# Kernel optimization log

Hardware: AMD Instinct MI355X
Metric: run time of the kernel (lower is better)

Reference implementation:

```python
import jax, jax.numpy as jnp
import numpy as np

N_NODES = 50000
N_EDGES = 1000000
HID = 64
L = 3
EPS_MSG = 1e-7   # GENConv message eps
EPS_SM = 1e-16   # PyG scatter-softmax denominator eps
LN_EPS = 1e-5


def layernorm(x, g, b):
    mu = jnp.mean(x, axis=-1, keepdims=True)
    var = jnp.var(x, axis=-1, keepdims=True)
    return (x - mu) * jax.lax.rsqrt(var + LN_EPS) * g + b


def genconv(x, src, dst, edge_attr, t, W1, b1, g1, be1, W2, b2):
    # message: relu(x_j + e_ij) + eps  -> [E, HID]
    msg = jax.nn.relu(x[src] + edge_attr) + EPS_MSG
    # softmax aggregation over incoming edges of each dst node
    logits = msg * t
    m = jax.ops.segment_max(logits, dst, num_segments=N_NODES)
    m = jnp.where(jnp.isfinite(m), m, 0.0)
    e = jnp.exp(logits - m[dst])
    s = jax.ops.segment_sum(e, dst, num_segments=N_NODES) + EPS_SM
    agg = jax.ops.segment_sum((e / s[dst]) * msg, dst, num_segments=N_NODES)
    # root residual + MLP [64 -> 128 -> 64]
    h = agg + x
    h = h @ W1 + b1
    h = jax.nn.relu(layernorm(h, g1, be1))
    return h @ W2 + b2


def setup_inputs() -> dict:
    key = jax.random.key(0)
    ks = jax.random.split(key, 10)
    inp = {
        'x': jax.random.normal(ks[0], (N_NODES, 16), jnp.float32),
        'edge_attr': jax.random.uniform(ks[1], (N_EDGES, 1), jnp.float32),
        'edge_index': jax.random.randint(ks[2], (2, N_EDGES), 0, N_NODES, jnp.int32),
        'W_node': jax.random.normal(ks[3], (16, HID), jnp.float32) / np.sqrt(16.0),
        'b_node': jnp.zeros((HID,), jnp.float32),
        'W_edge': jax.random.normal(ks[4], (1, HID), jnp.float32),
        'b_edge': jnp.zeros((HID,), jnp.float32),
        't': jnp.ones((L,), jnp.float32),
        'W1': jax.random.normal(ks[5], (L, HID, 2 * HID), jnp.float32) / np.sqrt(float(HID)),
        'b1': jnp.zeros((L, 2 * HID), jnp.float32),
        'ln_g': jnp.ones((L, 2 * HID), jnp.float32),
        'ln_b': jnp.zeros((L, 2 * HID), jnp.float32),
        'W2': jax.random.normal(ks[6], (L, 2 * HID, HID), jnp.float32) / np.sqrt(2.0 * HID),
        'b2': jnp.zeros((L, HID), jnp.float32),
        'norm_g': jnp.ones((L, HID), jnp.float32),
        'norm_b': jnp.zeros((L, HID), jnp.float32),
        'W_lin': jax.random.normal(ks[7], (HID, 64), jnp.float32) / np.sqrt(float(HID)),
        'b_lin': jnp.zeros((64,), jnp.float32),
    }
    return inp


def reference(x, edge_attr, edge_index, W_node, b_node, W_edge, b_edge, t,
              W1, b1, ln_g, ln_b, W2, b2, norm_g, norm_b, W_lin, b_lin):
    src, dst = edge_index[0], edge_index[1]
    h = x @ W_node + b_node                 # [N, HID]
    ea = edge_attr @ W_edge + b_edge        # [E, HID]
    # layer 0: conv only
    h = genconv(h, src, dst, ea, t[0], W1[0], b1[0], ln_g[0], ln_b[0], W2[0], b2[0])
    # layers 1..L-1: res+ blocks (norm -> relu -> conv -> residual); dropout is identity in eval
    for i in range(1, L):
        z = jax.nn.relu(layernorm(h, norm_g[i], norm_b[i]))
        h = h + genconv(z, src, dst, ea, t[i], W1[i], b1[i], ln_g[i], ln_b[i], W2[i], b2[i])
    # final norm/act reuses layer 0's norm
    h = jax.nn.relu(layernorm(h, norm_g[0], norm_b[0]))
    # adaptive avg/max pool (N, 64) -> (1, 32): pool over all nodes, channel bins of 2
    avg = h.mean(axis=0).reshape(32, 2).mean(axis=1)
    mx = h.max(axis=0).reshape(32, 2).max(axis=1)
    emb = jnp.concatenate([avg, mx])[None, :]   # [1, 64]
    return emb @ W_lin + b_lin                  # [1, 64]
```

## Files before the change

kernel.cpp:

```cpp
#include <hip/hip_runtime.h>
#include <math.h>

#define N_NODES 50000
#define N_EDGES 1000000
#define HID 64
#define SCAN_NB ((N_NODES + 1 + 255) / 256)
#define N_TILES (N_NODES / 16)
#define NB_MLP 512
#define NB2 64
#define VB_S 72
#define UB_S 136
static_assert(N_NODES % 16 == 0, "tile math");
static_assert(N_NODES <= 65536, "src must fit in 16 bits");

typedef __attribute__((ext_vector_type(8))) short short8;
typedef __attribute__((ext_vector_type(4))) float f32x4;

__device__ __forceinline__ unsigned short f2bf(float x) {
    unsigned u = __float_as_uint(x);
    u += 0x7FFFu + ((u >> 16) & 1u);
    return (unsigned short)(u >> 16);
}
__device__ __forceinline__ float bfbits_hi(unsigned pk) {
    return __uint_as_float(pk & 0xFFFF0000u);
}
__device__ __forceinline__ float bf2f(unsigned short v) {
    return __uint_as_float(((unsigned)v) << 16);
}
__device__ __forceinline__ unsigned addpk(unsigned a, unsigned b) {
    float lo = __uint_as_float(a << 16) + __uint_as_float(b << 16);
    float hi = __uint_as_float(a & 0xFFFF0000u) + __uint_as_float(b & 0xFFFF0000u);
    return (unsigned)f2bf(lo) | ((unsigned)f2bf(hi) << 16);
}

__global__ __launch_bounds__(256) void k_node_encode(
    const float* __restrict__ x, const float* __restrict__ Wn,
    const float* __restrict__ bn, unsigned short* __restrict__ zb) {
    int n = blockIdx.x * 4 + (threadIdx.x >> 6);
    int c = threadIdx.x & 63;
    if (n >= N_NODES) return;
    float acc = bn[c];
    const float* xr = x + n * 16;
    #pragma unroll
    for (int k = 0; k < 16; ++k) acc = fmaf(xr[k], Wn[k * 64 + c], acc);
    zb[n * 64 + c] = f2bf(acc);
}

__global__ __launch_bounds__(256) void k_wprep(
    const float* __restrict__ W1, const float* __restrict__ W2,
    unsigned short* __restrict__ w1p, unsigned short* __restrict__ w2p) {
    int i = blockIdx.x * 256 + threadIdx.x;
    if (i >= 3 * 8192) return;
    int L = i >> 13, r = i & 8191;
    int j = r & 7, lane = (r >> 3) & 63;
    int quad = lane >> 4, col = lane & 15;
    {
        int st = r >> 9;
        int s = st >> 3, t = st & 7;
        w1p[i] = f2bf(W1[L * 8192 + (s * 32 + quad * 8 + j) * 128 + t * 16 + col]);
    }
    {
        int ft = r >> 9;
        int s = ft >> 2, t = ft & 3;
        w2p[i] = f2bf(W2[L * 8192 + (s * 32 + quad * 8 + j) * 64 + t * 16 + col]);
    }
}

__global__ __launch_bounds__(256) void k_hist_rank(const int* __restrict__ ei,
                                                   int* __restrict__ cnt4, int* __restrict__ rank) {
    int i = blockIdx.x * blockDim.x + threadIdx.x;
    if (i >= N_EDGES) return;
    int c = i & 3;
    rank[i] = atomicAdd(&cnt4[c * N_NODES + ei[N_EDGES + i]], 1);
}

__global__ __launch_bounds__(256) void k_scan1(const int* __restrict__ cnt4,
                                               int* __restrict__ tot,
                                               int* __restrict__ inc, int* __restrict__ bsum) {
    __shared__ int sh[256];
    int gi = blockIdx.x * 256 + threadIdx.x;
    int v = 0;
    if (gi < N_NODES)
        v = cnt4[gi] + cnt4[N_NODES + gi] + cnt4[2 * N_NODES + gi] + cnt4[3 * N_NODES + gi];
    if (gi < N_NODES + 1) tot[gi] = v;
    sh[threadIdx.x] = v;
    __syncthreads();
    #pragma unroll
    for (int d = 1; d < 256; d <<= 1) {
        int t = (threadIdx.x >= d) ? sh[threadIdx.x - d] : 0;
        __syncthreads();
        sh[threadIdx.x] += t;
        __syncthreads();
    }
    if (gi < N_NODES + 1) inc[gi] = sh[threadIdx.x];
    if (threadIdx.x == 255) bsum[blockIdx.x] = sh[255];
}

__global__ __launch_bounds__(256) void k_scan2(int* __restrict__ bsum) {
    __shared__ int sh[256];
    int t = threadIdx.x;
    sh[t] = (t < SCAN_NB) ? bsum[t] : 0;
    __syncthreads();
    #pragma unroll
    for (int d = 1; d < 256; d <<= 1) {
        int v = (t >= d) ? sh[t - d] : 0;
        __syncthreads();
        sh[t] += v;
        __syncthreads();
    }
    if (t < SCAN_NB) bsum[t] = (t == 0) ? 0 : sh[t - 1];
}

__global__ __launch_bounds__(256) void k_scan3(const int* __restrict__ inc,
                                               const int* __restrict__ tot,
                                               const int* __restrict__ bsum,
                                               const int* __restrict__ cnt4,
                                               int* __restrict__ offs, int4* __restrict__ combined) {
    int gi = blockIdx.x * 256 + threadIdx.x;
    if (gi < N_NODES + 1) {
        int e = bsum[blockIdx.x] + inc[gi] - tot[gi];
        offs[gi] = e;
        if (gi < N_NODES) {
            int c0 = cnt4[gi], c1 = cnt4[N_NODES + gi], c2 = cnt4[2 * N_NODES + gi];
            combined[gi] = make_int4(e, e + c0, e + c0 + c1, e + c0 + c1 + c2);
        }
    }
}

__global__ __launch_bounds__(256) void k_scatter(
    const int* __restrict__ ei, const float* __restrict__ eattr,
    const int4* __restrict__ combined, const int* __restrict__ rank,
    unsigned int* __restrict__ s_pack) {
    int i = blockIdx.x * blockDim.x + threadIdx.x;
    if (i >= N_EDGES) return;
    int d = ei[N_EDGES + i];
    int c = i & 3;
    int4 cb = combined[d];
    int base = (c == 0) ? cb.x : (c == 1) ? cb.y : (c == 2) ? cb.z : cb.w;
    int p = base + rank[i];
    unsigned pk = ((unsigned)f2bf(eattr[i]) << 16) | (unsigned)(ei[i] & 0xFFFF);
    s_pack[p] = pk;
}

__global__ __launch_bounds__(256) void k_agg(
    const unsigned short* __restrict__ zb, const int* __restrict__ offs,
    const unsigned int* __restrict__ s_pack,
    const float* __restrict__ We, const float* __restrict__ be,
    const float* __restrict__ t, int layer, unsigned short* __restrict__ aggb) {
    int wid = (blockIdx.x * blockDim.x + threadIdx.x) >> 6;
    int lane = threadIdx.x & 63;
    if (wid >= N_NODES) return;
    int beg = offs[wid], end = offs[wid + 1];
    float we = We[lane], bev = be[lane];
    float tl = t[layer];
    float s = 0.f, num = 0.f;
    int i = beg;
    for (; i + 7 < end; i += 8) {
        unsigned pk[8];
        #pragma unroll
        for (int j = 0; j < 8; ++j) pk[j] = s_pack[i + j];
        float zv[8];
        #pragma unroll
        for (int j = 0; j < 8; ++j) zv[j] = bf2f(zb[(pk[j] & 0xFFFFu) * 64 + lane]);
        float acc_s = 0.f, acc_n = 0.f;
        #pragma unroll
        for (int j = 0; j < 8; ++j) {
            float msg = fmaxf(zv[j] + fmaf(bfbits_hi(pk[j]), we, bev), 0.f) + 1e-7f;
            float p = __expf(msg * tl);
            acc_s += p;
            acc_n = fmaf(p, msg, acc_n);
        }
        s += acc_s;
        num += acc_n;
    }
    for (; i < end; ++i) {
        unsigned pk = s_pack[i];
        float zz = bf2f(zb[(pk & 0xFFFFu) * 64 + lane]);
        float msg = fmaxf(zz + fmaf(bfbits_hi(pk), we, bev), 0.f) + 1e-7f;
        float p = __expf(msg * tl);
        s += p;
        num = fmaf(p, msg, num);
    }
    aggb[wid * 64 + lane] = f2bf(num / (s + 1e-16f));
}

__global__ __launch_bounds__(256) void k_mlp(
    const unsigned short* __restrict__ aggb, unsigned short* __restrict__ zb,
    unsigned short* __restrict__ hb,
    const unsigned short* __restrict__ w1p, const unsigned short* __restrict__ w2p,
    const float* __restrict__ b1,
    const float* __restrict__ g1, const float* __restrict__ be1,
    const float* __restrict__ b2,
    const float* __restrict__ ng, const float* __restrict__ nb, int mode,
    float* __restrict__ pb_sum, float* __restrict__ pb_max) {
    __shared__ unsigned short w1s[8192];
    __shared__ unsigned short w2s[8192];
    __shared__ unsigned short vbuf[4][16 * VB_S];
    __shared__ unsigned short ubuf[4][16 * UB_S];
    __shared__ float lssum[4][4][16], lsmax[4][4][16];
    int lane = threadIdx.x & 63;
    int wave = threadIdx.x >> 6;
    int col = lane & 15, quad = lane >> 4;
    unsigned short* vb = vbuf[wave];
    unsigned short* ub = ubuf[wave];

    {
        const uint4* s1 = (const uint4*)w1p;
        const uint4* s2 = (const uint4*)w2p;
        uint4* d1 = (uint4*)w1s;
        uint4* d2 = (uint4*)w2s;
        #pragma unroll
        for (int i = 0; i < 4; ++i) {
            d1[threadIdx.x + i * 256] = s1[threadIdx.x + i * 256];
            d2[threadIdx.x + i * 256] = s2[threadIdx.x + i * 256];
        }
    }
    __syncthreads();

    float b1f[8], g1f[8], e1f[8];
    #pragma unroll
    for (int t = 0; t < 8; ++t) {
        int ch = t * 16 + col;
        b1f[t] = b1[ch]; g1f[t] = g1[ch]; e1f[t] = be1[ch];
    }
    float b2f_[4], ngf[4], nbf[4];
    #pragma unroll
    for (int t = 0; t < 4; ++t) {
        b2f_[t] = b2[t * 16 + col];
        ngf[t] = ng[t * 16 + col];
        nbf[t] = nb[t * 16 + col];
    }

    float psum[4] = {0.f, 0.f, 0.f, 0.f};
    float pmax[4] = {0.f, 0.f, 0.f, 0.f};
    int nd = lane >> 2;
    int cg = (lane & 3) * 16;

    for (int tile = blockIdx.x * 4 + wave; tile < N_TILES; tile += NB_MLP * 4) {
        int n0 = tile * 16;
        const uint4* ap = (const uint4*)(aggb + (size_t)(n0 + nd) * 64 + cg);
        const uint4* zp = (const uint4*)(zb + (size_t)(n0 + nd) * 64 + cg);
        uint4 a0 = ap[0], a1 = ap[1], z0 = zp[0], z1 = zp[1];
        uint4 r0, r1;
        r0.x = addpk(a0.x, z0.x); r0.y = addpk(a0.y, z0.y);
        r0.z = addpk(a0.z, z0.z); r0.w = addpk(a0.w, z0.w);
        r1.x = addpk(a1.x, z1.x); r1.y = addpk(a1.y, z1.y);
        r1.z = addpk(a1.z, z1.z); r1.w = addpk(a1.w, z1.w);
        uint4* vdst = (uint4*)&vb[nd * VB_S + cg];
        vdst[0] = r0;
        vdst[1] = r1;

        short8 af0 = *(const short8*)&vb[col * VB_S + quad * 8];
        short8 af1 = *(const short8*)&vb[col * VB_S + 32 + quad * 8];

        uint4 h0, h1;
        if (mode >= 1) {
            const uint4* hp = (const uint4*)(hb + (size_t)(n0 + nd) * 64 + cg);
            h0 = hp[0]; h1 = hp[1];
        }

        f32x4 au[8];
        #pragma unroll
        for (int t = 0; t < 8; ++t) {
            short8 w0 = *(const short8*)&w1s[((0 * 8 + t) * 64 + lane) * 8];
            short8 w1 = *(const short8*)&w1s[((1 * 8 + t) * 64 + lane) * 8];
            f32x4 c = {0.f, 0.f, 0.f, 0.f};
            c = __builtin_amdgcn_mfma_f32_16x16x32_bf16(af0, w0, c, 0, 0, 0);
            c = __builtin_amdgcn_mfma_f32_16x16x32_bf16(af1, w1, c, 0, 0, 0);
            au[t] = c;
        }
        #pragma unroll
        for (int r = 0; r < 4; ++r) {
            float sx = 0.f, sq = 0.f;
            #pragma unroll
            for (int t = 0; t < 8; ++t) {
                float v = au[t][r] + b1f[t];
                sx += v; sq += v * v;
            }
            #pragma unroll
            for (int mask = 1; mask < 16; mask <<= 1) {
                sx += __shfl_xor(sx, mask, 64);
                sq += __shfl_xor(sq, mask, 64);
            }
            float mu = sx * (1.f / 128.f);
            float var = sq * (1.f / 128.f) - mu * mu;
            float rs = rsqrtf(var + 1e-5f);
            int row = quad * 4 + r;
            #pragma unroll
            for (int t = 0; t < 8; ++t) {
                float v = au[t][r] + b1f[t];
                float y = fmaxf(fmaf((v - mu) * rs, g1f[t], e1f[t]), 0.f);
                ub[row * UB_S + t * 16 + col] = f2bf(y);
            }
        }
        f32x4 oc[4];
        #pragma unroll
        for (int t = 0; t < 4; ++t) oc[t] = (f32x4){0.f, 0.f, 0.f, 0.f};
        #pragma unroll
        for (int s = 0; s < 4; ++s) {
            short8 a = *(const short8*)&ub[col * UB_S + s * 32 + quad * 8];
            #pragma unroll
            for (int t = 0; t < 4; ++t) {
                short8 w = *(const short8*)&w2s[((s * 4 + t) * 64 + lane) * 8];
                oc[t] = __builtin_amdgcn_mfma_f32_16x16x32_bf16(a, w, oc[t], 0, 0, 0);
            }
        }
        if (mode >= 1) {
            uint4* hdst = (uint4*)&vb[nd * VB_S + cg];
            hdst[0] = h0;
            hdst[1] = h1;
        }
        #pragma unroll
        for (int r = 0; r < 4; ++r) {
            int row = quad * 4 + r;
            float val[4];
            #pragma unroll
            for (int t = 0; t < 4; ++t) {
                val[t] = oc[t][r] + b2f_[t];
                if (mode >= 1) val[t] += bf2f(vb[row * VB_S + t * 16 + col]);
            }
            float sx = 0.f, sq = 0.f;
            #pragma unroll
            for (int t = 0; t < 4; ++t) { sx += val[t]; sq += val[t] * val[t]; }
            #pragma unroll
            for (int mask = 1; mask < 16; mask <<= 1) {
                sx += __shfl_xor(sx, mask, 64);
                sq += __shfl_xor(sq, mask, 64);
            }
            float mu = sx * (1.f / 64.f);
            float var = sq * (1.f / 64.f) - mu * mu;
            float rs = rsqrtf(var + 1e-5f);
            #pragma unroll
            for (int t = 0; t < 4; ++t) {
                float y = fmaxf(fmaf((val[t] - mu) * rs, ngf[t], nbf[t]), 0.f);
                if (mode <= 1) {
                    vb[row * VB_S + t * 16 + col] = f2bf(val[t]);
                    ub[row * UB_S + t * 16 + col] = f2bf(y);
                } else {
                    psum[t] += y;
                    pmax[t] = fmaxf(pmax[t], y);
                }
            }
        }
        if (mode <= 1) {
            const uint4* hsrc = (const uint4*)&vb[nd * VB_S + cg];
            const uint4* zsrc = (const uint4*)&ub[nd * UB_S + cg];
            uint4* hdst = (uint4*)(hb + (size_t)(n0 + nd) * 64 + cg);
            uint4* zdst = (uint4*)(zb + (size_t)(n0 + nd) * 64 + cg);
            hdst[0] = hsrc[0]; hdst[1] = hsrc[1];
            zdst[0] = zsrc[0]; zdst[1] = zsrc[1];
        }
    }
    if (mode == 2) {
        #pragma unroll
        for (int t = 0; t < 4; ++t) {
            psum[t] += __shfl_xor(psum[t], 16, 64);
            psum[t] += __shfl_xor(psum[t], 32, 64);
            pmax[t] = fmaxf(pmax[t], __shfl_xor(pmax[t], 16, 64));
            pmax[t] = fmaxf(pmax[t], __shfl_xor(pmax[t], 32, 64));
        }
        if (quad == 0) {
            #pragma unroll
            for (int t = 0; t < 4; ++t) {
                lssum[wave][t][col] = psum[t];
                lsmax[wave][t][col] = pmax[t];
            }
        }
        __syncthreads();
        if (wave == 0) {
            int t = lane >> 4, c = lane & 15;
            float s = lssum[0][t][c] + lssum[1][t][c] + lssum[2][t][c] + lssum[3][t][c];
            float mx = fmaxf(fmaxf(lsmax[0][t][c], lsmax[1][t][c]),
                             fmaxf(lsmax[2][t][c], lsmax[3][t][c]));
            pb_sum[blockIdx.x * 64 + lane] = s;
            pb_max[blockIdx.x * 64 + lane] = mx;
        }
    }
}

__global__ __launch_bounds__(256) void k_red(
    const float* __restrict__ pb_sum, const float* __restrict__ pb_max,
    float* __restrict__ p2_sum, float* __restrict__ p2_max) {
    __shared__ float sa4[4][64], sm4[4][64];
    int t = threadIdx.x;
    int ch = t & 63, part = t >> 6;
    float s = 0.f, mx = 0.f;
    for (int b = blockIdx.x + NB2 * part; b < NB_MLP; b += NB2 * 4) {
        s += pb_sum[b * 64 + ch];
        mx = fmaxf(mx, pb_max[b * 64 + ch]);
    }
    sa4[part][ch] = s; sm4[part][ch] = mx;
    __syncthreads();
    if (t < 64) {
        p2_sum[blockIdx.x * 64 + t] = sa4[0][t] + sa4[1][t] + sa4[2][t] + sa4[3][t];
        p2_max[blockIdx.x * 64 + t] =
            fmaxf(fmaxf(sm4[0][t], sm4[1][t]), fmaxf(sm4[2][t], sm4[3][t]));
    }
}

__global__ __launch_bounds__(256) void k_head(
    const float* __restrict__ p2_sum, const float* __restrict__ p2_max,
    const float* __restrict__ Wl, const float* __restrict__ bl, float* __restrict__ out) {
    __shared__ float sa4[4][64], sm4[4][64];
    __shared__ float sa[64], sm[64], emb[64];
    int t = threadIdx.x;
    int ch = t & 63, part = t >> 6;
    float s = 0.f, mx = 0.f;
    for (int b = part; b < NB2; b += 4) {
        s += p2_sum[b * 64 + ch];
        mx = fmaxf(mx, p2_max[b * 64 + ch]);
    }
    sa4[part][ch] = s; sm4[part][ch] = mx;
    __syncthreads();
    if (t < 64) {
        sa[t] = sa4[0][t] + sa4[1][t] + sa4[2][t] + sa4[3][t];
        sm[t] = fmaxf(fmaxf(sm4[0][t], sm4[1][t]), fmaxf(sm4[2][t], sm4[3][t]));
    }
    __syncthreads();
    if (t < 64) {
        if (t < 32) {
            emb[t] = (sa[2 * t] + sa[2 * t + 1]) * (0.5f / (float)N_NODES);
        } else {
            int i = t - 32;
            emb[t] = fmaxf(sm[2 * i], sm[2 * i + 1]);
        }
    }
    __syncthreads();
    if (t < 64) {
        float acc = bl[t];
        for (int k = 0; k < 64; ++k) acc = fmaf(emb[k], Wl[k * 64 + t], acc);
        out[t] = acc;
    }
}

extern "C" void kernel_launch(void* const* d_in, const int* in_sizes, int n_in,
                              void* d_out, int out_size, void* d_ws, size_t ws_size,
                              hipStream_t stream) {
    const float* x     = (const float*)d_in[0];
    const float* eattr = (const float*)d_in[1];
    const int*   ei    = (const int*)d_in[2];
    const float* Wn    = (const float*)d_in[3];
    const float* bn    = (const float*)d_in[4];
    const float* We    = (const float*)d_in[5];
    const float* be    = (const float*)d_in[6];
    const float* t     = (const float*)d_in[7];
    const float* W1    = (const float*)d_in[8];
    const float* b1    = (const float*)d_in[9];
    const float* lg    = (const float*)d_in[10];
    const float* lb    = (const float*)d_in[11];
    const float* W2    = (const float*)d_in[12];
    const float* b2    = (const float*)d_in[13];
    const float* ng    = (const float*)d_in[14];
    const float* nb    = (const float*)d_in[15];
    const float* Wl    = (const float*)d_in[16];
    const float* bl    = (const float*)d_in[17];
    float* out = (float*)d_out;

    char* p = (char*)d_ws;
    unsigned short* hb   = (unsigned short*)p; p += (size_t)N_NODES * 64 * 2;
    unsigned short* zb   = (unsigned short*)p; p += (size_t)N_NODES * 64 * 2;
    unsigned short* aggb = (unsigned short*)p; p += (size_t)N_NODES * 64 * 2;
    unsigned int* s_pack = (unsigned int*)p; p += (size_t)N_EDGES * 4;
    int* cnt4   = (int*)p;  p += (size_t)4 * N_NODES * 4;
    int* tot    = (int*)p;  p += (size_t)(N_NODES + 4) * 4;
    int* offs   = (int*)p;  p += (size_t)(N_NODES + 4) * 4;
    int* inc    = (int*)p;  p += (size_t)(N_NODES + 4) * 4;
    int* bsum   = (int*)p;  p += (size_t)256 * 4;
    int4* combined = (int4*)p; p += (size_t)N_NODES * 16;
    float* pb_sum = (float*)p; p += (size_t)NB_MLP * 64 * 4;
    float* pb_max = (float*)p; p += (size_t)NB_MLP * 64 * 4;
    float* p2_sum = (float*)p; p += (size_t)NB2 * 64 * 4;
    float* p2_max = (float*)p; p += (size_t)NB2 * 64 * 4;
    unsigned short* w1p = (unsigned short*)p; p += (size_t)3 * 8192 * 2;
    unsigned short* w2p = (unsigned short*)p; p += (size_t)3 * 8192 * 2;
    int* rank = (int*)p;    p += (size_t)N_EDGES * 4;

    hipMemsetAsync(cnt4, 0, (size_t)4 * N_NODES * sizeof(int), stream);

    k_node_encode<<<(N_NODES + 3) / 4, 256, 0, stream>>>(x, Wn, bn, zb);
    k_wprep<<<(3 * 8192 + 255) / 256, 256, 0, stream>>>(W1, W2, w1p, w2p);
    k_hist_rank<<<(N_EDGES + 255) / 256, 256, 0, stream>>>(ei, cnt4, rank);
    k_scan1<<<SCAN_NB, 256, 0, stream>>>(cnt4, tot, inc, bsum);
    k_scan2<<<1, 256, 0, stream>>>(bsum);
    k_scan3<<<SCAN_NB, 256, 0, stream>>>(inc, tot, bsum, cnt4, offs, combined);
    k_scatter<<<(N_EDGES + 255) / 256, 256, 0, stream>>>(ei, eattr, combined, rank, s_pack);

    k_agg<<<(N_NODES + 3) / 4, 256, 0, stream>>>(zb, offs, s_pack, We, be, t, 0, aggb);
    k_mlp<<<NB_MLP, 256, 0, stream>>>(aggb, zb, hb, w1p, w2p, b1, lg, lb, b2,
                                      ng + 64, nb + 64, 0, pb_sum, pb_max);
    k_agg<<<(N_NODES + 3) / 4, 256, 0, stream>>>(zb, offs, s_pack, We, be, t, 1, aggb);
    k_mlp<<<NB_MLP, 256, 0, stream>>>(aggb, zb, hb, w1p + 8192, w2p + 8192,
                                      b1 + 128, lg + 128, lb + 128, b2 + 64,
                                      ng + 128, nb + 128, 1, pb_sum, pb_max);
    k_agg<<<(N_NODES + 3) / 4, 256, 0, stream>>>(zb, offs, s_pack, We, be, t, 2, aggb);
    k_mlp<<<NB_MLP, 256, 0, stream>>>(aggb, zb, hb, w1p + 2 * 8192, w2p + 2 * 8192,
                                      b1 + 2 * 128, lg + 2 * 128, lb + 2 * 128, b2 + 2 * 64,
                                      ng, nb, 2, pb_sum, pb_max);

    k_red<<<NB2, 256, 0, stream>>>(pb_sum, pb_max, p2_sum, p2_max);
    k_head<<<1, 256, 0, stream>>>(p2_sum, p2_max, Wl, bl, out);
}
```

Before: 352.0 us.

## Fuse front kernels, scan stages, pooling reduce; vectorize agg gather over channel pairs

Merges node encoding, weight packing and the edge histogram into one launch, folds the block-sum scan into the final scan kernel, and merges the two-stage pooling reduction into a single 1024-thread head kernel. The aggregation kernel now has each lane process two channels via 32-bit bf16-pair loads, with the two half-waves handling alternating edges and combining through a cross-half shuffle. This reduces launch overhead and per-edge gather instruction count, at the cost of redundant scan work per block and a single-block final reduction.

```diff
diff --git a/kernel.cpp b/kernel.cpp
--- a/kernel.cpp
+++ b/kernel.cpp
@@ -7,9 +7,11 @@
 #define SCAN_NB ((N_NODES + 1 + 255) / 256)
 #define N_TILES (N_NODES / 16)
 #define NB_MLP 512
-#define NB2 64
 #define VB_S 72
 #define UB_S 136
+#define NB_ENC ((N_NODES + 3) / 4)
+#define NB_WPREP ((3 * 8192 + 255) / 256)
+#define NB_HIST ((N_EDGES + 255) / 256)
 static_assert(N_NODES % 16 == 0, "tile math");
 static_assert(N_NODES <= 65536, "src must fit in 16 bits");
 
@@ -33,45 +35,44 @@
     return (unsigned)f2bf(lo) | ((unsigned)f2bf(hi) << 16);
 }
 
-__global__ __launch_bounds__(256) void k_node_encode(
+__global__ __launch_bounds__(256) void k_front(
     const float* __restrict__ x, const float* __restrict__ Wn,
-    const float* __restrict__ bn, unsigned short* __restrict__ zb) {
-    int n = blockIdx.x * 4 + (threadIdx.x >> 6);
-    int c = threadIdx.x & 63;
-    if (n >= N_NODES) return;
-    float acc = bn[c];
-    const float* xr = x + n * 16;
-    #pragma unroll
-    for (int k = 0; k < 16; ++k) acc = fmaf(xr[k], Wn[k * 64 + c], acc);
-    zb[n * 64 + c] = f2bf(acc);
-}
-
-__global__ __launch_bounds__(256) void k_wprep(
+    const float* __restrict__ bn, unsigned short* __restrict__ zb,
     const float* __restrict__ W1, const float* __restrict__ W2,
-    unsigned short* __restrict__ w1p, unsigned short* __restrict__ w2p) {
-    int i = blockIdx.x * 256 + threadIdx.x;
-    if (i >= 3 * 8192) return;
-    int L = i >> 13, r = i & 8191;
-    int j = r & 7, lane = (r >> 3) & 63;
-    int quad = lane >> 4, col = lane & 15;
-    {
-        int st = r >> 9;
-        int s = st >> 3, t = st & 7;
-        w1p[i] = f2bf(W1[L * 8192 + (s * 32 + quad * 8 + j) * 128 + t * 16 + col]);
-    }
-    {
-        int ft = r >> 9;
-        int s = ft >> 2, t = ft & 3;
-        w2p[i] = f2bf(W2[L * 8192 + (s * 32 + quad * 8 + j) * 64 + t * 16 + col]);
-    }
-}
-
-__global__ __launch_bounds__(256) void k_hist_rank(const int* __restrict__ ei,
-                                                   int* __restrict__ cnt4, int* __restrict__ rank) {
-    int i = blockIdx.x * blockDim.x + threadIdx.x;
-    if (i >= N_EDGES) return;
-    int c = i & 3;
-    rank[i] = atomicAdd(&cnt4[c * N_NODES + ei[N_EDGES + i]], 1);
+    unsigned short* __restrict__ w1p, unsigned short* __restrict__ w2p,
+    const int* __restrict__ ei, int* __restrict__ cnt4, int* __restrict__ rank) {
+    int b = blockIdx.x;
+    if (b < NB_ENC) {
+        int n = b * 4 + (threadIdx.x >> 6);
+        int c = threadIdx.x & 63;
+        if (n >= N_NODES) return;
+        float acc = bn[c];
+        const float* xr = x + n * 16;
+        #pragma unroll
+        for (int k = 0; k < 16; ++k) acc = fmaf(xr[k], Wn[k * 64 + c], acc);
+        zb[n * 64 + c] = f2bf(acc);
+    } else if (b < NB_ENC + NB_WPREP) {
+        int i = (b - NB_ENC) * 256 + threadIdx.x;
+        if (i >= 3 * 8192) return;
+        int L = i >> 13, r = i & 8191;
+        int j = r & 7, lane = (r >> 3) & 63;
+        int quad = lane >> 4, col = lane & 15;
+        {
+            int st = r >> 9;
+            int s = st >> 3, t = st & 7;
+            w1p[i] = f2bf(W1[L * 8192 + (s * 32 + quad * 8 + j) * 128 + t * 16 + col]);
+        }
+        {
+            int ft = r >> 9;
+            int s = ft >> 2, t = ft & 3;
+            w2p[i] = f2bf(W2[L * 8192 + (s * 32 + quad * 8 + j) * 64 + t * 16 + col]);
+        }
+    } else {
+        int i = (b - NB_ENC - NB_WPREP) * 256 + threadIdx.x;
+        if (i >= N_EDGES) return;
+        int c = i & 3;
+        rank[i] = atomicAdd(&cnt4[c * N_NODES + ei[N_EDGES + i]], 1);
+    }
 }
 
 __global__ __launch_bounds__(256) void k_scan1(const int* __restrict__ cnt4,
@@ -96,7 +97,11 @@
     if (threadIdx.x == 255) bsum[blockIdx.x] = sh[255];
 }
 
-__global__ __launch_bounds__(256) void k_scan2(int* __restrict__ bsum) {
+__global__ __launch_bounds__(256) void k_scan3(const int* __restrict__ inc,
+                                               const int* __restrict__ tot,
+                                               const int* __restrict__ bsum,
+                                               const int* __restrict__ cnt4,
+                                               int* __restrict__ offs, int4* __restrict__ combined) {
     __shared__ int sh[256];
     int t = threadIdx.x;
     sh[t] = (t < SCAN_NB) ? bsum[t] : 0;
@@ -108,17 +113,10 @@
         sh[t] += v;
         __syncthreads();
     }
-    if (t < SCAN_NB) bsum[t] = (t == 0) ? 0 : sh[t - 1];
-}
-
-__global__ __launch_bounds__(256) void k_scan3(const int* __restrict__ inc,
-                                               const int* __restrict__ tot,
-                                               const int* __restrict__ bsum,
-                                               const int* __restrict__ cnt4,
-                                               int* __restrict__ offs, int4* __restrict__ combined) {
-    int gi = blockIdx.x * 256 + threadIdx.x;
+    int base = (blockIdx.x == 0) ? 0 : sh[blockIdx.x - 1];
+    int gi = blockIdx.x * 256 + t;
     if (gi < N_NODES + 1) {
-        int e = bsum[blockIdx.x] + inc[gi] - tot[gi];
+        int e = base + inc[gi] - tot[gi];
         offs[gi] = e;
         if (gi < N_NODES) {
             int c0 = cnt4[gi], c1 = cnt4[N_NODES + gi], c2 = cnt4[2 * N_NODES + gi];
@@ -151,37 +149,71 @@
     int lane = threadIdx.x & 63;
     if (wid >= N_NODES) return;
     int beg = offs[wid], end = offs[wid + 1];
-    float we = We[lane], bev = be[lane];
+    int half = lane >> 5;
+    int c2 = lane & 31;
+    float we0 = We[2 * c2], we1 = We[2 * c2 + 1];
+    float bv0 = be[2 * c2], bv1 = be[2 * c2 + 1];
     float tl = t[layer];
-    float s = 0.f, num = 0.f;
+    const unsigned* zbu = (const unsigned*)zb;
+    float s0 = 0.f, s1 = 0.f, n0 = 0.f, n1 = 0.f;
     int i = beg;
     for (; i + 7 < end; i += 8) {
-        unsigned pk[8];
-        #pragma unroll
-        for (int j = 0; j < 8; ++j) pk[j] = s_pack[i + j];
-        float zv[8];
-        #pragma unroll
-        for (int j = 0; j < 8; ++j) zv[j] = bf2f(zb[(pk[j] & 0xFFFFu) * 64 + lane]);
-        float acc_s = 0.f, acc_n = 0.f;
-        #pragma unroll
-        for (int j = 0; j < 8; ++j) {
-            float msg = fmaxf(zv[j] + fmaf(bfbits_hi(pk[j]), we, bev), 0.f) + 1e-7f;
-            float p = __expf(msg * tl);
-            acc_s += p;
-            acc_n = fmaf(p, msg, acc_n);
-        }
-        s += acc_s;
-        num += acc_n;
-    }
-    for (; i < end; ++i) {
+        unsigned pk[4];
+        #pragma unroll
+        for (int j = 0; j < 4; ++j) {
+            unsigned pa = s_pack[i + 2 * j];
+            unsigned pb = s_pack[i + 2 * j + 1];
+            pk[j] = half ? pb : pa;
+        }
+        unsigned zu[4];
+        #pragma unroll
+        for (int j = 0; j < 4; ++j) zu[j] = zbu[(pk[j] & 0xFFFFu) * 32 + c2];
+        #pragma unroll
+        for (int j = 0; j < 4; ++j) {
+            float ea = bfbits_hi(pk[j]);
+            float z0 = __uint_as_float(zu[j] << 16);
+            float z1 = __uint_as_float(zu[j] & 0xFFFF0000u);
+            float m0 = fmaxf(z0 + fmaf(ea, we0, bv0), 0.f) + 1e-7f;
+            float m1 = fmaxf(z1 + fmaf(ea, we1, bv1), 0.f) + 1e-7f;
+            float p0 = __expf(m0 * tl), p1 = __expf(m1 * tl);
+            s0 += p0; n0 = fmaf(p0, m0, n0);
+            s1 += p1; n1 = fmaf(p1, m1, n1);
+        }
+    }
+    for (; i + 1 < end; i += 2) {
+        unsigned pa = s_pack[i], pb = s_pack[i + 1];
+        unsigned pk = half ? pb : pa;
+        unsigned zu = zbu[(pk & 0xFFFFu) * 32 + c2];
+        float ea = bfbits_hi(pk);
+        float z0 = __uint_as_float(zu << 16);
+        float z1 = __uint_as_float(zu & 0xFFFF0000u);
+        float m0 = fmaxf(z0 + fmaf(ea, we0, bv0), 0.f) + 1e-7f;
+        float m1 = fmaxf(z1 + fmaf(ea, we1, bv1), 0.f) + 1e-7f;
+        float p0 = __expf(m0 * tl), p1 = __expf(m1 * tl);
+        s0 += p0; n0 = fmaf(p0, m0, n0);
+        s1 += p1; n1 = fmaf(p1, m1, n1);
+    }
+    if (i < end) {
         unsigned pk = s_pack[i];
-        float zz = bf2f(zb[(pk & 0xFFFFu) * 64 + lane]);
-        float msg = fmaxf(zz + fmaf(bfbits_hi(pk), we, bev), 0.f) + 1e-7f;
-        float p = __expf(msg * tl);
-        s += p;
-        num = fmaf(p, msg, num);
-    }
-    aggb[wid * 64 + lane] = f2bf(num / (s + 1e-16f));
+        unsigned zu = zbu[(pk & 0xFFFFu) * 32 + c2];
+        float ea = bfbits_hi(pk);
+        float z0 = __uint_as_float(zu << 16);
+        float z1 = __uint_as_float(zu & 0xFFFF0000u);
+        float m0 = fmaxf(z0 + fmaf(ea, we0, bv0), 0.f) + 1e-7f;
+        float m1 = fmaxf(z1 + fmaf(ea, we1, bv1), 0.f) + 1e-7f;
+        float p0 = __expf(m0 * tl), p1 = __expf(m1 * tl);
+        if (half == 0) {
+            s0 += p0; n0 = fmaf(p0, m0, n0);
+            s1 += p1; n1 = fmaf(p1, m1, n1);
+        }
+    }
+    s0 += __shfl_xor(s0, 32, 64); n0 += __shfl_xor(n0, 32, 64);
+    s1 += __shfl_xor(s1, 32, 64); n1 += __shfl_xor(n1, 32, 64);
+    if (half == 0) {
+        unsigned r = (unsigned)f2bf(n0 / (s0 + 1e-16f)) |
+                     ((unsigned)f2bf(n1 / (s1 + 1e-16f)) << 16);
+        ((unsigned*)aggb)[wid * 32 + c2] = r;
+    }
 }
 
 __global__ __launch_bounds__(256) void k_mlp(
@@ -378,43 +410,28 @@
     }
 }
 
-__global__ __launch_bounds__(256) void k_red(
+__global__ __launch_bounds__(1024) void k_head(
     const float* __restrict__ pb_sum, const float* __restrict__ pb_max,
-    float* __restrict__ p2_sum, float* __restrict__ p2_max) {
-    __shared__ float sa4[4][64], sm4[4][64];
-    int t = threadIdx.x;
-    int ch = t & 63, part = t >> 6;
-    float s = 0.f, mx = 0.f;
-    for (int b = blockIdx.x + NB2 * part; b < NB_MLP; b += NB2 * 4) {
-        s += pb_sum[b * 64 + ch];
-        mx = fmaxf(mx, pb_max[b * 64 + ch]);
-    }
-    sa4[part][ch] = s; sm4[part][ch] = mx;
-    __syncthreads();
-    if (t < 64) {
-        p2_sum[blockIdx.x * 64 + t] = sa4[0][t] + sa4[1][t] + sa4[2][t] + sa4[3][t];
-        p2_max[blockIdx.x * 64 + t] =
-            fmaxf(fmaxf(sm4[0][t], sm4[1][t]), fmaxf(sm4[2][t], sm4[3][t]));
-    }
-}
-
-__global__ __launch_bounds__(256) void k_head(
-    const float* __restrict__ p2_sum, const float* __restrict__ p2_max,
     const float* __restrict__ Wl, const float* __restrict__ bl, float* __restrict__ out) {
-    __shared__ float sa4[4][64], sm4[4][64];
+    __shared__ float sa4[16][64], sm4[16][64];
     __shared__ float sa[64], sm[64], emb[64];
     int t = threadIdx.x;
     int ch = t & 63, part = t >> 6;
     float s = 0.f, mx = 0.f;
-    for (int b = part; b < NB2; b += 4) {
-        s += p2_sum[b * 64 + ch];
-        mx = fmaxf(mx, p2_max[b * 64 + ch]);
+    for (int b = part; b < NB_MLP; b += 16) {
+        s += pb_sum[b * 64 + ch];
+        mx = fmaxf(mx, pb_max[b * 64 + ch]);
     }
     sa4[part][ch] = s; sm4[part][ch] = mx;
     __syncthreads();
     if (t < 64) {
-        sa[t] = sa4[0][t] + sa4[1][t] + sa4[2][t] + sa4[3][t];
-        sm[t] = fmaxf(fmaxf(sm4[0][t], sm4[1][t]), fmaxf(sm4[2][t], sm4[3][t]));
+        float ss = 0.f, mm = 0.f;
+        #pragma unroll
+        for (int q = 0; q < 16; ++q) {
+            ss += sa4[q][t];
+            mm = fmaxf(mm, sm4[q][t]);
+        }
+        sa[t] = ss; sm[t] = mm;
     }
     __syncthreads();
     if (t < 64) {
@@ -469,19 +486,15 @@
     int4* combined = (int4*)p; p += (size_t)N_NODES * 16;
     float* pb_sum = (float*)p; p += (size_t)NB_MLP * 64 * 4;
     float* pb_max = (float*)p; p += (size_t)NB_MLP * 64 * 4;
-    float* p2_sum = (float*)p; p += (size_t)NB2 * 64 * 4;
-    float* p2_max = (float*)p; p += (size_t)NB2 * 64 * 4;
     unsigned short* w1p = (unsigned short*)p; p += (size_t)3 * 8192 * 2;
     unsigned short* w2p = (unsigned short*)p; p += (size_t)3 * 8192 * 2;
     int* rank = (int*)p;    p += (size_t)N_EDGES * 4;
 
     hipMemsetAsync(cnt4, 0, (size_t)4 * N_NODES * sizeof(int), stream);
 
-    k_node_encode<<<(N_NODES + 3) / 4, 256, 0, stream>>>(x, Wn, bn, zb);
-    k_wprep<<<(3 * 8192 + 255) / 256, 256, 0, stream>>>(W1, W2, w1p, w2p);
-    k_hist_rank<<<(N_EDGES + 255) / 256, 256, 0, stream>>>(ei, cnt4, rank);
+    k_front<<<NB_ENC + NB_WPREP + NB_HIST, 256, 0, stream>>>(
+        x, Wn, bn, zb, W1, W2, w1p, w2p, ei, cnt4, rank);
     k_scan1<<<SCAN_NB, 256, 0, stream>>>(cnt4, tot, inc, bsum);
-    k_scan2<<<1, 256, 0, stream>>>(bsum);
     k_scan3<<<SCAN_NB, 256, 0, stream>>>(inc, tot, bsum, cnt4, offs, combined);
     k_scatter<<<(N_EDGES + 255) / 256, 256, 0, stream>>>(ei, eattr, combined, rank, s_pack);
 
@@ -497,6 +510,5 @@
                                       b1 + 2 * 128, lg + 2 * 128, lb + 2 * 128, b2 + 2 * 64,
                                       ng, nb, 2, pb_sum, pb_max);
 
-    k_red<<<NB2, 256, 0, stream>>>(pb_sum, pb_max, p2_sum, p2_max);
-    k_head<<<1, 256, 0, stream>>>(p2_sum, p2_max, Wl, bl, out);
-}
+    k_head<<<1, 1024, 0, stream>>>(pb_sum, pb_max, Wl, bl, out);
+}
```

Result: faster. 330.4 us (-6.1%).
